# Kernel optimization log

Measured on AMD Instinct MI355X. Metric: run time of the kernel, lower is better.

Reference implementation:

```python
import jax, jax.numpy as jnp
import numpy as np

K = 2  # top-k experts per token


def setup_inputs() -> dict:
    key = jax.random.key(0)
    k1, k2, k3, k4 = jax.random.split(key, 4)
    B, S, D, E = 4, 4096, 1024, 64
    x = jax.random.normal(k1, (B, S, D), dtype=jnp.float32)
    gate_w = jax.random.normal(k2, (E, D), dtype=jnp.float32) * (1.0 / np.sqrt(D))
    noise_weight = jax.random.normal(k3, (E,), dtype=jnp.float32) * 0.02
    noise = jax.random.normal(k4, (B, S, E), dtype=jnp.float32)  # randn_like(logits) * noisy_std(=1.0)
    return {"x": x, "gate_w": gate_w, "noise_weight": noise_weight, "noise": noise}


def reference(x, gate_w, noise_weight, noise):
    E = gate_w.shape[0]
    # logits = x @ W^T  -> [B, S, E]
    logits = jnp.einsum("bsd,ed->bse", x, gate_w)
    logits_noisy = logits + noise * noise_weight  # noisy_std = 1.0 folded into `noise`
    top_vals, top_idx = jax.lax.top_k(logits_noisy, K)  # [B,S,K]
    # scatter top-k logits into a -inf mask, then softmax over experts
    keep = jax.nn.one_hot(top_idx, E, dtype=jnp.bool_).any(axis=-2)  # [B,S,E]
    neg_inf = jnp.finfo(logits_noisy.dtype).min
    sparse = jnp.where(keep, logits_noisy, neg_inf)
    weights = jax.nn.softmax(sparse, axis=-1)
    return weights, top_idx
```

## Files before the change

kernel.cpp:

```cpp
#include <hip/hip_runtime.h>
#include <math.h>


#define DDIM 1024
#define NEXP 64
#define NTOK 16384

typedef float f4 __attribute__((ext_vector_type(4)));
typedef short s8 __attribute__((ext_vector_type(8)));
typedef unsigned int u32;

static __device__ __forceinline__ void split3(float f, short& h, short& m, short& l) {
    const u32 uf = __float_as_uint(f);
    h = (short)(uf >> 16);
    const float r1 = f - __uint_as_float(uf & 0xffff0000u);
    const u32 u1 = __float_as_uint(r1);
    m = (short)(u1 >> 16);
    const float r2 = r1 - __uint_as_float(u1 & 0xffff0000u);
    l = (short)(__float_as_uint(r2) >> 16);
}

__global__ __launch_bounds__(256)
void w_prep(const float* __restrict__ gw, short* __restrict__ wimg) {
    const int uid = blockIdx.x * 256 + threadIdx.x;
    const int c   = uid >> 9;
    const int kk  = (uid >> 8) & 1;
    const int e   = (uid >> 2) & 63;
    const int q   = uid & 3;
    const int k0  = c * 64 + kk * 32 + q * 8;
    const float* src = gw + (size_t)e * DDIM + k0;
    s8 hv, mv, lv;
    #pragma unroll
    for (int j = 0; j < 8; ++j) {
        short h, m, l;
        split3(src[j], h, m, l);
        hv[j] = h; mv[j] = m; lv[j] = l;
    }
    const size_t base = (size_t)c * 1536 + (kk * 3) * 256
                      + (e >> 4) * 64 + q * 16 + (e & 15);
    *(s8*)(wimg + (base      ) * 8) = hv;
    *(s8*)(wimg + (base + 256) * 8) = mv;
    *(s8*)(wimg + (base + 512) * 8) = lv;
}

static __device__ __forceinline__ u32 packhi(float flo, float fhi) {
    return __builtin_amdgcn_perm(__float_as_uint(fhi), __float_as_uint(flo),
                                 0x07060302u);
}

union FragU { u32 u[4]; s8 v; };

static __device__ __forceinline__ void conv8(const float* f, s8& h, s8& m, s8& l) {
    FragU H, M, L;
    #pragma unroll
    for (int j = 0; j < 4; ++j) {
        const float f0 = f[2 * j], f1 = f[2 * j + 1];
        H.u[j] = packhi(f0, f1);
        const float g0 = f0 - __uint_as_float(__float_as_uint(f0) & 0xffff0000u);
        const float g1 = f1 - __uint_as_float(__float_as_uint(f1) & 0xffff0000u);
        M.u[j] = packhi(g0, g1);
        const float e0 = g0 - __uint_as_float(__float_as_uint(g0) & 0xffff0000u);
        const float e1 = g1 - __uint_as_float(__float_as_uint(g1) & 0xffff0000u);
        L.u[j] = packhi(e0, e1);
    }
    h = H.v; m = M.v; l = L.v;
}

#define MF(A, B, C) __builtin_amdgcn_mfma_f32_16x16x32_bf16((A), (B), (C), 0, 0, 0)

#define LOADA(S, P) { const float* _a = (P);                \
    S[0] = *(const f4*)(_a);      S[1] = *(const f4*)(_a + 4);  \
    S[2] = *(const f4*)(_a + 32); S[3] = *(const f4*)(_a + 36); }

#define LOADB(B, P) { const short* _b = (P);                \
    B[0] = *(const s8*)(_b);         B[1] = *(const s8*)(_b + 2048); \
    B[2] = *(const s8*)(_b + 4096);  B[3] = *(const s8*)(_b + 6144); \
    B[4] = *(const s8*)(_b + 8192);  B[5] = *(const s8*)(_b + 10240); }

#define PART(SA, SB, NC)                                              \
  {                                                                   \
    s8 ah0, am0, al0, ah1, am1, al1;                                  \
    conv8((const float*)&SA[0], ah0, am0, al0);                       \
    conv8((const float*)&SA[2], ah1, am1, al1);                       \
    if ((NC) < 16) LOADA(SA, xrow + (NC) * 64);                       \
    acc0 = MF(ah0, SB[0], acc0);  acc1 = MF(ah0, SB[1], acc1);        \
    acc1 = MF(am0, SB[0], acc1);  acc1 = MF(ah0, SB[2], acc1);        \
    acc1 = MF(am0, SB[1], acc1);  acc1 = MF(al0, SB[0], acc1);        \
    acc0 = MF(ah1, SB[3], acc0);  acc1 = MF(ah1, SB[4], acc1);        \
    acc1 = MF(am1, SB[3], acc1);  acc1 = MF(ah1, SB[5], acc1);        \
    acc1 = MF(am1, SB[4], acc1);  acc1 = MF(al1, SB[3], acc1);        \
    if ((NC) < 16) LOADB(SB, wb + (size_t)(NC) * 12288);              \
    __builtin_amdgcn_sched_barrier(0);                                \
  }

__global__ __launch_bounds__(256, 3)
void gate_fused(const float* __restrict__ x,
                const short* __restrict__ wimg,
                const float* __restrict__ noise_weight,
                const float* __restrict__ noise,
                float* __restrict__ out_w,
                float* __restrict__ out_i)
{
    __shared__ float Lds[16][66];

    const int tid  = threadIdx.x;
    const int lane = tid & 63;
    const int wv   = tid >> 6;
    const int m    = lane & 15;
    const int q    = lane >> 4;
    const int tokBase = blockIdx.x * 16;

    const float* xrow = x + (size_t)(tokBase + m) * DDIM + q * 8;
    const short* wb   = wimg + ((size_t)wv * 64 + lane) * 8;

    const float nw = noise_weight[lane];
    float nz[4];
    #pragma unroll
    for (int tt = 0; tt < 4; ++tt)
        nz[tt] = noise[(size_t)(tokBase + wv * 4 + tt) * NEXP + lane];

    f4 acc0 = (f4)0.f, acc1 = (f4)0.f;

    f4 sa0[4], sa1[4];
    s8 b0[6], b1[6];

    LOADA(sa0, xrow);           LOADB(b0, wb);
    LOADA(sa1, xrow + 64);      LOADB(b1, wb + 12288);
    __builtin_amdgcn_sched_barrier(0);

    #pragma unroll
    for (int cc = 0; cc < 16; cc += 2) {
        PART(sa0, b0, cc + 2);
        PART(sa1, b1, cc + 3);
    }

    #pragma unroll
    for (int r = 0; r < 4; ++r)
        Lds[q * 4 + r][m + 16 * wv] = acc0[r] + acc1[r];
    __syncthreads();

    #pragma unroll
    for (int tt = 0; tt < 4; ++tt) {
        const int tok  = wv * 4 + tt;
        const int gtok = tokBase + tok;
        const float ln = fmaf(nz[tt], nw, Lds[tok][lane]);

        float v1 = ln; int i1 = lane;
        #pragma unroll
        for (int off = 32; off > 0; off >>= 1) {
            const float vo = __shfl_xor(v1, off, 64);
            const int   io = __shfl_xor(i1, off, 64);
            if (vo > v1 || (vo == v1 && io < i1)) { v1 = vo; i1 = io; }
        }
        float v2 = (lane == i1) ? -3.4e38f : ln; int i2 = lane;
        #pragma unroll
        for (int off = 32; off > 0; off >>= 1) {
            const float vo = __shfl_xor(v2, off, 64);
            const int   io = __shfl_xor(i2, off, 64);
            if (vo > v2 || (vo == v2 && io < i2)) { v2 = vo; i2 = io; }
        }

        const float d   = expf(v2 - v1);
        const float inv = 1.f / (1.f + d);
        const float wgt = (lane == i1) ? inv : ((lane == i2) ? d * inv : 0.f);
        out_w[(size_t)gtok * NEXP + lane] = wgt;
        if (lane == 0) {
            out_i[(size_t)gtok * 2]     = (float)i1;
            out_i[(size_t)gtok * 2 + 1] = (float)i2;
        }
    }
}

extern "C" void kernel_launch(void* const* d_in, const int* in_sizes, int n_in,
                              void* d_out, int out_size, void* d_ws, size_t ws_size,
                              hipStream_t stream) {
    const float* x     = (const float*)d_in[0];
    const float* gw    = (const float*)d_in[1];
    const float* nwt   = (const float*)d_in[2];
    const float* noise = (const float*)d_in[3];
    float* out_w = (float*)d_out;
    float* out_i = (float*)d_out + (size_t)NTOK * NEXP;

    short* wimg = (short*)d_ws;

    hipLaunchKernelGGL(w_prep, dim3(32), dim3(256), 0, stream, gw, wimg);
    hipLaunchKernelGGL(gate_fused, dim3(NTOK / 16), dim3(256), 0, stream,
                       x, wimg, nwt, noise, out_w, out_i);
}
```

Before: 144.5 us.

## Stage gate weights in LDS via async global-to-LDS loads, 32 tokens per block

```diff
diff --git a/kernel.cpp b/kernel.cpp
--- a/kernel.cpp
+++ b/kernel.cpp
@@ -18,6 +18,12 @@
     m = (short)(u1 >> 16);
     const float r2 = r1 - __uint_as_float(u1 & 0xffff0000u);
     l = (short)(__float_as_uint(r2) >> 16);
+}
+
+static __device__ __forceinline__ void gl_lds16(const void* g, void* l) {
+    __builtin_amdgcn_global_load_lds(
+        (const __attribute__((address_space(1))) u32*)g,
+        (__attribute__((address_space(3))) u32*)l, 16, 0, 0);
 }
 
 __global__ __launch_bounds__(256)
@@ -68,32 +74,7 @@
 
 #define MF(A, B, C) __builtin_amdgcn_mfma_f32_16x16x32_bf16((A), (B), (C), 0, 0, 0)
 
-#define LOADA(S, P) { const float* _a = (P);                \
-    S[0] = *(const f4*)(_a);      S[1] = *(const f4*)(_a + 4);  \
-    S[2] = *(const f4*)(_a + 32); S[3] = *(const f4*)(_a + 36); }
-
-#define LOADB(B, P) { const short* _b = (P);                \
-    B[0] = *(const s8*)(_b);         B[1] = *(const s8*)(_b + 2048); \
-    B[2] = *(const s8*)(_b + 4096);  B[3] = *(const s8*)(_b + 6144); \
-    B[4] = *(const s8*)(_b + 8192);  B[5] = *(const s8*)(_b + 10240); }
-
-#define PART(SA, SB, NC)                                              \
-  {                                                                   \
-    s8 ah0, am0, al0, ah1, am1, al1;                                  \
-    conv8((const float*)&SA[0], ah0, am0, al0);                       \
-    conv8((const float*)&SA[2], ah1, am1, al1);                       \
-    if ((NC) < 16) LOADA(SA, xrow + (NC) * 64);                       \
-    acc0 = MF(ah0, SB[0], acc0);  acc1 = MF(ah0, SB[1], acc1);        \
-    acc1 = MF(am0, SB[0], acc1);  acc1 = MF(ah0, SB[2], acc1);        \
-    acc1 = MF(am0, SB[1], acc1);  acc1 = MF(al0, SB[0], acc1);        \
-    acc0 = MF(ah1, SB[3], acc0);  acc1 = MF(ah1, SB[4], acc1);        \
-    acc1 = MF(am1, SB[3], acc1);  acc1 = MF(ah1, SB[5], acc1);        \
-    acc1 = MF(am1, SB[4], acc1);  acc1 = MF(al1, SB[3], acc1);        \
-    if ((NC) < 16) LOADB(SB, wb + (size_t)(NC) * 12288);              \
-    __builtin_amdgcn_sched_barrier(0);                                \
-  }
-
-__global__ __launch_bounds__(256, 3)
+__global__ __launch_bounds__(256, 2)
 void gate_fused(const float* __restrict__ x,
                 const short* __restrict__ wimg,
                 const float* __restrict__ noise_weight,
@@ -101,47 +82,109 @@
                 float* __restrict__ out_w,
                 float* __restrict__ out_i)
 {
-    __shared__ float Lds[16][66];
+    __shared__ short bs[2][1536 * 8];
+    __shared__ float Lds[32][66];
 
     const int tid  = threadIdx.x;
     const int lane = tid & 63;
     const int wv   = tid >> 6;
     const int m    = lane & 15;
     const int q    = lane >> 4;
-    const int tokBase = blockIdx.x * 16;
-
-    const float* xrow = x + (size_t)(tokBase + m) * DDIM + q * 8;
-    const short* wb   = wimg + ((size_t)wv * 64 + lane) * 8;
+    const int ts   = wv & 1;
+    const int eh   = wv >> 1;
+    const int tokBase = blockIdx.x * 32;
+
+    const float* xrow = x + (size_t)(tokBase + ts * 16 + m) * DDIM + q * 8;
+    const int t64a = (eh * 2 + 0) * 64;
+    const int t64b = (eh * 2 + 1) * 64;
 
     const float nw = noise_weight[lane];
-    float nz[4];
-    #pragma unroll
-    for (int tt = 0; tt < 4; ++tt)
-        nz[tt] = noise[(size_t)(tokBase + wv * 4 + tt) * NEXP + lane];
-
-    f4 acc0 = (f4)0.f, acc1 = (f4)0.f;
+    float nz[8];
+    #pragma unroll
+    for (int tt = 0; tt < 8; ++tt)
+        nz[tt] = noise[(size_t)(tokBase + wv * 8 + tt) * NEXP + lane];
+
+    f4 accA0 = (f4)0.f, accB0 = (f4)0.f;
+    f4 accA1 = (f4)0.f, accB1 = (f4)0.f;
 
     f4 sa0[4], sa1[4];
-    s8 b0[6], b1[6];
-
-    LOADA(sa0, xrow);           LOADB(b0, wb);
-    LOADA(sa1, xrow + 64);      LOADB(b1, wb + 12288);
-    __builtin_amdgcn_sched_barrier(0);
-
-    #pragma unroll
-    for (int cc = 0; cc < 16; cc += 2) {
-        PART(sa0, b0, cc + 2);
-        PART(sa1, b1, cc + 3);
-    }
-
-    #pragma unroll
-    for (int r = 0; r < 4; ++r)
-        Lds[q * 4 + r][m + 16 * wv] = acc0[r] + acc1[r];
+
+#define STAGE(BUF, C) {                                              \
+    const short* _c = wimg + (size_t)(C) * 12288;                    \
+    _Pragma("unroll")                                                \
+    for (int _i = 0; _i < 6; ++_i) {                                 \
+        const int _off = (wv * 6 + _i) * 512;                        \
+        gl_lds16(_c + _off + lane * 8, &bs[BUF][_off]);              \
+    } }
+
+#define LOADA(S, C) { const float* _a = xrow + (C) * 64;             \
+    S[0] = *(const f4*)(_a);      S[1] = *(const f4*)(_a + 4);       \
+    S[2] = *(const f4*)(_a + 32); S[3] = *(const f4*)(_a + 36); }
+
+#define COMPUTE(BUF, SA) {                                           \
+    s8 ah0, am0, al0, ah1, am1, al1;                                 \
+    conv8((const float*)&SA[0], ah0, am0, al0);                      \
+    conv8((const float*)&SA[2], ah1, am1, al1);                      \
+    { const int p = t64a + lane;                                     \
+      const s8 bh = *(const s8*)&bs[BUF][(p       ) * 8];            \
+      const s8 bm = *(const s8*)&bs[BUF][(p +  256) * 8];            \
+      const s8 bl = *(const s8*)&bs[BUF][(p +  512) * 8];            \
+      accA0 = MF(ah0, bh, accA0);  accB0 = MF(ah0, bm, accB0);       \
+      accB0 = MF(am0, bh, accB0);  accB0 = MF(ah0, bl, accB0);       \
+      accB0 = MF(am0, bm, accB0);  accB0 = MF(al0, bh, accB0); }     \
+    { const int p = t64b + lane;                                     \
+      const s8 bh = *(const s8*)&bs[BUF][(p       ) * 8];            \
+      const s8 bm = *(const s8*)&bs[BUF][(p +  256) * 8];            \
+      const s8 bl = *(const s8*)&bs[BUF][(p +  512) * 8];            \
+      accA1 = MF(ah0, bh, accA1);  accB1 = MF(ah0, bm, accB1);       \
+      accB1 = MF(am0, bh, accB1);  accB1 = MF(ah0, bl, accB1);       \
+      accB1 = MF(am0, bm, accB1);  accB1 = MF(al0, bh, accB1); }     \
+    { const int p = 768 + t64a + lane;                               \
+      const s8 bh = *(const s8*)&bs[BUF][(p       ) * 8];            \
+      const s8 bm = *(const s8*)&bs[BUF][(p +  256) * 8];            \
+      const s8 bl = *(const s8*)&bs[BUF][(p +  512) * 8];            \
+      accA0 = MF(ah1, bh, accA0);  accB0 = MF(ah1, bm, accB0);       \
+      accB0 = MF(am1, bh, accB0);  accB0 = MF(ah1, bl, accB0);       \
+      accB0 = MF(am1, bm, accB0);  accB0 = MF(al1, bh, accB0); }     \
+    { const int p = 768 + t64b + lane;                               \
+      const s8 bh = *(const s8*)&bs[BUF][(p       ) * 8];            \
+      const s8 bm = *(const s8*)&bs[BUF][(p +  256) * 8];            \
+      const s8 bl = *(const s8*)&bs[BUF][(p +  512) * 8];            \
+      accA1 = MF(ah1, bh, accA1);  accB1 = MF(ah1, bm, accB1);       \
+      accB1 = MF(am1, bh, accB1);  accB1 = MF(ah1, bl, accB1);       \
+      accB1 = MF(am1, bm, accB1);  accB1 = MF(al1, bh, accB1); }     \
+  }
+
+    STAGE(0, 0);
+    LOADA(sa0, 0);
+
+    #pragma unroll
+    for (int c = 0; c < 16; c += 2) {
+        __syncthreads();
+        STAGE(1, c + 1);
+        LOADA(sa1, c + 1);
+        __builtin_amdgcn_sched_barrier(0);
+        COMPUTE(0, sa0);
+
+        __syncthreads();
+        if (c + 2 < 16) {
+            STAGE(0, c + 2);
+            LOADA(sa0, c + 2);
+        }
+        __builtin_amdgcn_sched_barrier(0);
+        COMPUTE(1, sa1);
+    }
+
+    #pragma unroll
+    for (int r = 0; r < 4; ++r) {
+        Lds[ts * 16 + q * 4 + r][m + 16 * (eh * 2 + 0)] = accA0[r] + accB0[r];
+        Lds[ts * 16 + q * 4 + r][m + 16 * (eh * 2 + 1)] = accA1[r] + accB1[r];
+    }
     __syncthreads();
 
     #pragma unroll
-    for (int tt = 0; tt < 4; ++tt) {
-        const int tok  = wv * 4 + tt;
+    for (int tt = 0; tt < 8; ++tt) {
+        const int tok  = wv * 8 + tt;
         const int gtok = tokBase + tok;
         const float ln = fmaf(nz[tt], nw, Lds[tok][lane]);
 
@@ -184,6 +227,6 @@
     short* wimg = (short*)d_ws;
 
     hipLaunchKernelGGL(w_prep, dim3(32), dim3(256), 0, stream, gw, wimg);
-    hipLaunchKernelGGL(gate_fused, dim3(NTOK / 16), dim3(256), 0, stream,
+    hipLaunchKernelGGL(gate_fused, dim3(NTOK / 32), dim3(256), 0, stream,
                        x, wimg, nwt, noise, out_w, out_i);
 }
```

New measurement: 126.8 us. 12.2% less time.

## Split K across waves with 64-token blocks and LDS reduction of partials

Applied to the files above, without the earlier changes.

```diff
diff --git a/kernel.cpp b/kernel.cpp
--- a/kernel.cpp
+++ b/kernel.cpp
@@ -68,32 +68,7 @@
 
 #define MF(A, B, C) __builtin_amdgcn_mfma_f32_16x16x32_bf16((A), (B), (C), 0, 0, 0)
 
-#define LOADA(S, P) { const float* _a = (P);                \
-    S[0] = *(const f4*)(_a);      S[1] = *(const f4*)(_a + 4);  \
-    S[2] = *(const f4*)(_a + 32); S[3] = *(const f4*)(_a + 36); }
-
-#define LOADB(B, P) { const short* _b = (P);                \
-    B[0] = *(const s8*)(_b);         B[1] = *(const s8*)(_b + 2048); \
-    B[2] = *(const s8*)(_b + 4096);  B[3] = *(const s8*)(_b + 6144); \
-    B[4] = *(const s8*)(_b + 8192);  B[5] = *(const s8*)(_b + 10240); }
-
-#define PART(SA, SB, NC)                                              \
-  {                                                                   \
-    s8 ah0, am0, al0, ah1, am1, al1;                                  \
-    conv8((const float*)&SA[0], ah0, am0, al0);                       \
-    conv8((const float*)&SA[2], ah1, am1, al1);                       \
-    if ((NC) < 16) LOADA(SA, xrow + (NC) * 64);                       \
-    acc0 = MF(ah0, SB[0], acc0);  acc1 = MF(ah0, SB[1], acc1);        \
-    acc1 = MF(am0, SB[0], acc1);  acc1 = MF(ah0, SB[2], acc1);        \
-    acc1 = MF(am0, SB[1], acc1);  acc1 = MF(al0, SB[0], acc1);        \
-    acc0 = MF(ah1, SB[3], acc0);  acc1 = MF(ah1, SB[4], acc1);        \
-    acc1 = MF(am1, SB[3], acc1);  acc1 = MF(ah1, SB[5], acc1);        \
-    acc1 = MF(am1, SB[4], acc1);  acc1 = MF(al1, SB[3], acc1);        \
-    if ((NC) < 16) LOADB(SB, wb + (size_t)(NC) * 12288);              \
-    __builtin_amdgcn_sched_barrier(0);                                \
-  }
-
-__global__ __launch_bounds__(256, 3)
+__global__ __launch_bounds__(256, 1)
 void gate_fused(const float* __restrict__ x,
                 const short* __restrict__ wimg,
                 const float* __restrict__ noise_weight,
@@ -101,49 +76,83 @@
                 float* __restrict__ out_w,
                 float* __restrict__ out_i)
 {
-    __shared__ float Lds[16][66];
+    __shared__ float Lsum[4][64][68];
 
     const int tid  = threadIdx.x;
     const int lane = tid & 63;
     const int wv   = tid >> 6;
     const int m    = lane & 15;
     const int q    = lane >> 4;
-    const int tokBase = blockIdx.x * 16;
+    const int tokBase = blockIdx.x * 64;
 
-    const float* xrow = x + (size_t)(tokBase + m) * DDIM + q * 8;
-    const short* wb   = wimg + ((size_t)wv * 64 + lane) * 8;
+    f4 a0[4][4], a1[4][4];
+    #pragma unroll
+    for (int mt = 0; mt < 4; ++mt)
+        #pragma unroll
+        for (int t = 0; t < 4; ++t) { a0[mt][t] = (f4)0.f; a1[mt][t] = (f4)0.f; }
 
-    const float nw = noise_weight[lane];
-    float nz[4];
-    #pragma unroll
-    for (int tt = 0; tt < 4; ++tt)
-        nz[tt] = noise[(size_t)(tokBase + wv * 4 + tt) * NEXP + lane];
-
-    f4 acc0 = (f4)0.f, acc1 = (f4)0.f;
-
-    f4 sa0[4], sa1[4];
-    s8 b0[6], b1[6];
-
-    LOADA(sa0, xrow);           LOADB(b0, wb);
-    LOADA(sa1, xrow + 64);      LOADB(b1, wb + 12288);
-    __builtin_amdgcn_sched_barrier(0);
+    const short* wbase = wimg + (size_t)(wv * 4) * 12288;
+    const float* xbase = x + (size_t)(tokBase + m) * DDIM + wv * 256 + q * 8;
 
     #pragma unroll
-    for (int cc = 0; cc < 16; cc += 2) {
-        PART(sa0, b0, cc + 2);
-        PART(sa1, b1, cc + 3);
+    for (int j = 0; j < 4; ++j) {
+        #pragma unroll
+        for (int kk = 0; kk < 2; ++kk) {
+            const short* bp = wbase + (size_t)j * 12288 + kk * 3 * 2048;
+            s8 B[12];
+            #pragma unroll
+            for (int t = 0; t < 4; ++t)
+                #pragma unroll
+                for (int lv = 0; lv < 3; ++lv)
+                    B[t * 3 + lv] = *(const s8*)(bp + ((size_t)lv * 256 + t * 64 + lane) * 8);
+
+            #pragma unroll
+            for (int mt = 0; mt < 4; ++mt) {
+                const float* ap = xbase + (size_t)mt * 16 * DDIM + j * 64 + kk * 32;
+                const f4 x0 = *(const f4*)(ap);
+                const f4 x1 = *(const f4*)(ap + 4);
+                float xf[8];
+                #pragma unroll
+                for (int i = 0; i < 4; ++i) { xf[i] = x0[i]; xf[4 + i] = x1[i]; }
+                s8 ah, am_, al;
+                conv8(xf, ah, am_, al);
+                #pragma unroll
+                for (int t = 0; t < 4; ++t) {
+                    const s8 bh = B[t * 3], bm = B[t * 3 + 1], bl = B[t * 3 + 2];
+                    a0[mt][t] = MF(ah,  bh, a0[mt][t]);
+                    a1[mt][t] = MF(ah,  bm, a1[mt][t]);
+                    a1[mt][t] = MF(am_, bh, a1[mt][t]);
+                    a1[mt][t] = MF(ah,  bl, a1[mt][t]);
+                    a1[mt][t] = MF(am_, bm, a1[mt][t]);
+                    a1[mt][t] = MF(al,  bh, a1[mt][t]);
+                }
+            }
+        }
     }
 
     #pragma unroll
-    for (int r = 0; r < 4; ++r)
-        Lds[q * 4 + r][m + 16 * wv] = acc0[r] + acc1[r];
+    for (int mt = 0; mt < 4; ++mt)
+        #pragma unroll
+        for (int t = 0; t < 4; ++t)
+            #pragma unroll
+            for (int r = 0; r < 4; ++r)
+                Lsum[wv][mt * 16 + q * 4 + r][t * 16 + m] = a0[mt][t][r] + a1[mt][t][r];
+
+    const float nw = noise_weight[lane];
+    float nz[16];
+    #pragma unroll
+    for (int tt = 0; tt < 16; ++tt)
+        nz[tt] = noise[(size_t)(tokBase + wv * 16 + tt) * NEXP + lane];
+
     __syncthreads();
 
     #pragma unroll
-    for (int tt = 0; tt < 4; ++tt) {
-        const int tok  = wv * 4 + tt;
+    for (int tt = 0; tt < 16; ++tt) {
+        const int tok  = wv * 16 + tt;
         const int gtok = tokBase + tok;
-        const float ln = fmaf(nz[tt], nw, Lds[tok][lane]);
+        const float ln = fmaf(nz[tt], nw,
+                              (Lsum[0][tok][lane] + Lsum[1][tok][lane]) +
+                              (Lsum[2][tok][lane] + Lsum[3][tok][lane]));
 
         float v1 = ln; int i1 = lane;
         #pragma unroll
@@ -184,6 +193,6 @@
     short* wimg = (short*)d_ws;
 
     hipLaunchKernelGGL(w_prep, dim3(32), dim3(256), 0, stream, gw, wimg);
-    hipLaunchKernelGGL(gate_fused, dim3(NTOK / 16), dim3(256), 0, stream,
+    hipLaunchKernelGGL(gate_fused, dim3(NTOK / 64), dim3(256), 0, stream,
                        x, wimg, nwt, noise, out_w, out_i);
 }
```

After: 138.9 us. 3.8% less time.

## Stage x and weight chunks through LDS with direct global-to-LDS loads, 32-token tiles

Applied to the files above, without the earlier changes.

```diff
diff --git a/kernel.cpp b/kernel.cpp
--- a/kernel.cpp
+++ b/kernel.cpp
@@ -18,6 +18,12 @@
     m = (short)(u1 >> 16);
     const float r2 = r1 - __uint_as_float(u1 & 0xffff0000u);
     l = (short)(__float_as_uint(r2) >> 16);
+}
+
+static __device__ __forceinline__ void gl_lds16(const void* g, void* l) {
+    __builtin_amdgcn_global_load_lds(
+        (const __attribute__((address_space(1))) u32*)g,
+        (__attribute__((address_space(3))) u32*)l, 16, 0, 0);
 }
 
 __global__ __launch_bounds__(256)
@@ -68,32 +74,7 @@
 
 #define MF(A, B, C) __builtin_amdgcn_mfma_f32_16x16x32_bf16((A), (B), (C), 0, 0, 0)
 
-#define LOADA(S, P) { const float* _a = (P);                \
-    S[0] = *(const f4*)(_a);      S[1] = *(const f4*)(_a + 4);  \
-    S[2] = *(const f4*)(_a + 32); S[3] = *(const f4*)(_a + 36); }
-
-#define LOADB(B, P) { const short* _b = (P);                \
-    B[0] = *(const s8*)(_b);         B[1] = *(const s8*)(_b + 2048); \
-    B[2] = *(const s8*)(_b + 4096);  B[3] = *(const s8*)(_b + 6144); \
-    B[4] = *(const s8*)(_b + 8192);  B[5] = *(const s8*)(_b + 10240); }
-
-#define PART(SA, SB, NC)                                              \
-  {                                                                   \
-    s8 ah0, am0, al0, ah1, am1, al1;                                  \
-    conv8((const float*)&SA[0], ah0, am0, al0);                       \
-    conv8((const float*)&SA[2], ah1, am1, al1);                       \
-    if ((NC) < 16) LOADA(SA, xrow + (NC) * 64);                       \
-    acc0 = MF(ah0, SB[0], acc0);  acc1 = MF(ah0, SB[1], acc1);        \
-    acc1 = MF(am0, SB[0], acc1);  acc1 = MF(ah0, SB[2], acc1);        \
-    acc1 = MF(am0, SB[1], acc1);  acc1 = MF(al0, SB[0], acc1);        \
-    acc0 = MF(ah1, SB[3], acc0);  acc1 = MF(ah1, SB[4], acc1);        \
-    acc1 = MF(am1, SB[3], acc1);  acc1 = MF(ah1, SB[5], acc1);        \
-    acc1 = MF(am1, SB[4], acc1);  acc1 = MF(al1, SB[3], acc1);        \
-    if ((NC) < 16) LOADB(SB, wb + (size_t)(NC) * 12288);              \
-    __builtin_amdgcn_sched_barrier(0);                                \
-  }
-
-__global__ __launch_bounds__(256, 3)
+__global__ __launch_bounds__(256, 2)
 void gate_fused(const float* __restrict__ x,
                 const short* __restrict__ wimg,
                 const float* __restrict__ noise_weight,
@@ -101,49 +82,104 @@
                 float* __restrict__ out_w,
                 float* __restrict__ out_i)
 {
-    __shared__ float Lds[16][66];
+    __shared__ short bs[2][1536 * 8];
+    __shared__ float xs[2][32 * 64];
 
     const int tid  = threadIdx.x;
     const int lane = tid & 63;
     const int wv   = tid >> 6;
+    const int es   = wv & 1;
+    const int kh   = wv >> 1;
     const int m    = lane & 15;
     const int q    = lane >> 4;
-    const int tokBase = blockIdx.x * 16;
-
-    const float* xrow = x + (size_t)(tokBase + m) * DDIM + q * 8;
-    const short* wb   = wimg + ((size_t)wv * 64 + lane) * 8;
+    const int tokBase = blockIdx.x * 32;
 
     const float nw = noise_weight[lane];
-    float nz[4];
-    #pragma unroll
-    for (int tt = 0; tt < 4; ++tt)
-        nz[tt] = noise[(size_t)(tokBase + wv * 4 + tt) * NEXP + lane];
-
-    f4 acc0 = (f4)0.f, acc1 = (f4)0.f;
-
-    f4 sa0[4], sa1[4];
-    s8 b0[6], b1[6];
-
-    LOADA(sa0, xrow);           LOADB(b0, wb);
-    LOADA(sa1, xrow + 64);      LOADB(b1, wb + 12288);
-    __builtin_amdgcn_sched_barrier(0);
-
-    #pragma unroll
-    for (int cc = 0; cc < 16; cc += 2) {
-        PART(sa0, b0, cc + 2);
-        PART(sa1, b1, cc + 3);
-    }
-
-    #pragma unroll
-    for (int r = 0; r < 4; ++r)
-        Lds[q * 4 + r][m + 16 * wv] = acc0[r] + acc1[r];
+    float nz[8];
+    #pragma unroll
+    for (int tt = 0; tt < 8; ++tt)
+        nz[tt] = noise[(size_t)(tokBase + wv * 8 + tt) * NEXP + lane];
+
+    f4 acc0[2][2], acc1[2][2];
+    #pragma unroll
+    for (int a = 0; a < 2; ++a)
+        #pragma unroll
+        for (int b = 0; b < 2; ++b) { acc0[a][b] = (f4)0.f; acc1[a][b] = (f4)0.f; }
+
+#define STAGE(BUF, C) {                                                    \
+    const short* _c = wimg + (size_t)(C) * 12288;                          \
+    _Pragma("unroll")                                                      \
+    for (int _i = 0; _i < 6; ++_i) {                                       \
+        const int _off = (wv * 6 + _i) * 512;                              \
+        gl_lds16(_c + _off + lane * 8, &bs[BUF][_off]);                    \
+    }                                                                      \
+    _Pragma("unroll")                                                      \
+    for (int _j = 0; _j < 2; ++_j) {                                       \
+        const int _qi = (wv * 2 + _j) * 64 + lane;                         \
+        const int _tk = _qi >> 4;                                          \
+        const int _qd = (_qi & 15) ^ (_tk & 15);                           \
+        gl_lds16(x + (size_t)(tokBase + _tk) * DDIM + (C) * 64 + _qd * 4,  \
+                 &xs[BUF][(wv * 2 + _j) * 256]);                           \
+    } }
+
+#define COMPUTE(BUF) {                                                     \
+    s8 ah[2], am_[2], al[2];                                               \
+    _Pragma("unroll")                                                      \
+    for (int mt = 0; mt < 2; ++mt) {                                       \
+        const int tok = mt * 16 + m;                                       \
+        const int qd0 = kh * 8 + q * 2;                                    \
+        const int sq0 = qd0 ^ (tok & 15);                                  \
+        const int sq1 = (qd0 + 1) ^ (tok & 15);                            \
+        const f4 xa = *(const f4*)&xs[BUF][tok * 64 + sq0 * 4];            \
+        const f4 xb = *(const f4*)&xs[BUF][tok * 64 + sq1 * 4];            \
+        float xf[8];                                                       \
+        _Pragma("unroll")                                                  \
+        for (int i = 0; i < 4; ++i) { xf[i] = xa[i]; xf[4 + i] = xb[i]; }  \
+        conv8(xf, ah[mt], am_[mt], al[mt]);                                \
+    }                                                                      \
+    _Pragma("unroll")                                                      \
+    for (int tt = 0; tt < 2; ++tt) {                                       \
+        const int p = (kh * 3) * 256 + (es * 2 + tt) * 64 + lane;          \
+        const s8 bh = *(const s8*)&bs[BUF][(p      ) * 8];                 \
+        const s8 bm = *(const s8*)&bs[BUF][(p + 256) * 8];                 \
+        const s8 bl = *(const s8*)&bs[BUF][(p + 512) * 8];                 \
+        _Pragma("unroll")                                                  \
+        for (int mt = 0; mt < 2; ++mt) {                                   \
+            acc0[mt][tt] = MF(ah[mt],  bh, acc0[mt][tt]);                  \
+            acc1[mt][tt] = MF(ah[mt],  bm, acc1[mt][tt]);                  \
+            acc1[mt][tt] = MF(am_[mt], bh, acc1[mt][tt]);                  \
+            acc1[mt][tt] = MF(ah[mt],  bl, acc1[mt][tt]);                  \
+            acc1[mt][tt] = MF(am_[mt], bm, acc1[mt][tt]);                  \
+            acc1[mt][tt] = MF(al[mt],  bh, acc1[mt][tt]);                  \
+        }                                                                  \
+    } }
+
+    STAGE(0, 0);
+
+    #pragma unroll
+    for (int c = 0; c < 16; ++c) {
+        __syncthreads();
+        if (c + 1 < 16) STAGE((c + 1) & 1, c + 1);
+        COMPUTE(c & 1);
+    }
+
+    float (*Lsum)[32][68] = reinterpret_cast<float(*)[32][68]>(&bs[0][0]);
+    #pragma unroll
+    for (int mt = 0; mt < 2; ++mt)
+        #pragma unroll
+        for (int tt = 0; tt < 2; ++tt)
+            #pragma unroll
+            for (int r = 0; r < 4; ++r)
+                Lsum[kh][mt * 16 + q * 4 + r][(es * 2 + tt) * 16 + m]
+                    = acc0[mt][tt][r] + acc1[mt][tt][r];
     __syncthreads();
 
     #pragma unroll
-    for (int tt = 0; tt < 4; ++tt) {
-        const int tok  = wv * 4 + tt;
+    for (int tt = 0; tt < 8; ++tt) {
+        const int tok  = wv * 8 + tt;
         const int gtok = tokBase + tok;
-        const float ln = fmaf(nz[tt], nw, Lds[tok][lane]);
+        const float ln = fmaf(nz[tt], nw,
+                              Lsum[0][tok][lane] + Lsum[1][tok][lane]);
 
         float v1 = ln; int i1 = lane;
         #pragma unroll
@@ -184,6 +220,6 @@
     short* wimg = (short*)d_ws;
 
     hipLaunchKernelGGL(w_prep, dim3(32), dim3(256), 0, stream, gw, wimg);
-    hipLaunchKernelGGL(gate_fused, dim3(NTOK / 16), dim3(256), 0, stream,
+    hipLaunchKernelGGL(gate_fused, dim3(NTOK / 32), dim3(256), 0, stream,
                        x, wimg, nwt, noise, out_w, out_i);
 }
```

Result: faster. 125.8 us (-12.9%).
